# Kernel optimization log

Hardware: AMD Instinct MI355X
Metric: run time of the kernel (lower is better)

Reference implementation:

```python
import jax, jax.numpy as jnp
import numpy as np

B, FIN, FOUT, FH2, NMIX, LAT, H, W = 16, 256, 256, 256, 8, 512, 64, 64


def _xavier(key, shape):
    # xavier_normal_ over last-two-ish dims; simple fan-based scale
    fan_in = int(np.prod(shape[1:]))
    fan_out = shape[0]
    s = (2.0 / (fan_in + fan_out)) ** 0.5
    return jax.random.normal(key, shape, jnp.float32) * s


def setup_inputs() -> dict:
    key = jax.random.key(0)
    ks = jax.random.split(key, 12)
    return {
        "x": jax.random.normal(ks[0], (B, FIN, H, W), jnp.float32),
        "lat": jax.random.normal(ks[1], (B, LAT), jnp.float32),
        # mixture kernel banks [n_mix, out_ch, in_ch] (kernel_size=1 squeezed)
        "k_in_mix": _xavier(ks[2], (NMIX, FH2, FIN)),
        "k_mid_mix": _xavier(ks[3], (NMIX, FH2, 2 * FH2)),
        "k_out_mix": _xavier(ks[4], (NMIX, FOUT, 2 * FH2)),
        "k_short_mix": _xavier(ks[5], (NMIX, FOUT, FIN)),
        # mixture bias banks [n_mix, ch]
        "b_in_mix": _xavier(ks[6], (NMIX, FH2)),
        "b_mid_mix": _xavier(ks[7], (NMIX, FH2)),
        "b_out_mix": _xavier(ks[8], (NMIX, FOUT)),
        "b_short_mix": _xavier(ks[9], (NMIX, FOUT)),
        # dyna_mix = nn.Linear(lat_size, n_mix) (lat_factor=0 path)
        "w_dyna": _xavier(ks[10], (NMIX, LAT)),
        "b_dyna": jnp.zeros((NMIX,), jnp.float32),
    }


def _complex_wave(h):
    # doubles channel dim: concat(sin, cos) along channels (per sample)
    return jnp.concatenate([jnp.sin(h), jnp.cos(h)], axis=1)


def reference(x, lat, k_in_mix, k_mid_mix, k_out_mix, k_short_mix,
              b_in_mix, b_mid_mix, b_out_mix, b_short_mix, w_dyna, b_dyna):
    # mixing coefficients per sample: [B, n_mix]
    mix = lat @ w_dyna.T + b_dyna
    # per-sample 1x1 conv kernels via mixture reduction: [B, out, in]
    k_in = jnp.einsum('bm,moi->boi', mix, k_in_mix)
    k_mid = jnp.einsum('bm,moi->boi', mix, k_mid_mix)
    k_out = jnp.einsum('bm,moi->boi', mix, k_out_mix)
    k_short = jnp.einsum('bm,moi->boi', mix, k_short_mix)
    # per-sample biases: [B, ch, 1, 1]
    b_in = (mix @ b_in_mix)[:, :, None, None]
    b_mid = (mix @ b_mid_mix)[:, :, None, None]
    b_out = (mix @ b_out_mix)[:, :, None, None]
    b_short = (mix @ b_short_mix)[:, :, None, None]
    # grouped conv with groups = batch (kernel_size=1) == per-sample matmul
    short = jnp.einsum('boi,bihw->bohw', k_short, x) + b_short
    h = jnp.einsum('boi,bihw->bohw', k_in, x) + b_in            # [B, FH2, H, W]
    h = _complex_wave(h)                                        # [B, 2*FH2, H, W]
    h = jnp.einsum('boi,bihw->bohw', k_mid, h) + b_mid
    h = _complex_wave(h)
    out = jnp.einsum('boi,bihw->bohw', k_out, h) + b_out + short
    return out
```

## Files before the change

### kernel.cpp

```cpp
#include <hip/hip_runtime.h>
#include <stdint.h>

#define B_    16
#define FIN   256
#define FOUT  256
#define FH2   256
#define NMIX  8
#define LAT   512
#define HW    4096
#define MT    64

typedef short bf16x8 __attribute__((ext_vector_type(8)));
typedef float f32x4  __attribute__((ext_vector_type(4)));

#define WS_MIX    0
#define WS_BIAS   1024
#define WS_WIN    131072
#define WS_WMID   2228224
#define WS_WOUT   6422528
#define WS_WSHORT 10616832

__device__ __forceinline__ uint16_t f2bf(float f) {
  uint32_t u = __builtin_bit_cast(uint32_t, f);
  u += 0x7fffu + ((u >> 16) & 1u);
  return (uint16_t)(u >> 16);
}
__device__ __forceinline__ uint32_t pack2(float lo, float hi) {
  return (uint32_t)f2bf(lo) | ((uint32_t)f2bf(hi) << 16);
}

#define MFMA(a, b, c) __builtin_amdgcn_mfma_f32_16x16x32_bf16(a, b, c, 0, 0, 0)

__global__ void k_mix_bias(const float* __restrict__ lat,
                           const float* __restrict__ w_dyna,
                           const float* __restrict__ b_dyna,
                           const float* __restrict__ b_in_mix,
                           const float* __restrict__ b_mid_mix,
                           const float* __restrict__ b_out_mix,
                           const float* __restrict__ b_short_mix,
                           float* __restrict__ ws_mix,
                           float* __restrict__ ws_bias) {
  __shared__ float smix[NMIX];
  const int t = threadIdx.x;
  const int lane = t & 63, wv = t >> 6;
  const int b = blockIdx.x;
#pragma unroll
  for (int d2 = 0; d2 < 2; d2++) {
    int m = wv * 2 + d2;
    float s = 0.f;
#pragma unroll
    for (int j = 0; j < 8; j++)
      s += lat[b * LAT + j * 64 + lane] * w_dyna[m * LAT + j * 64 + lane];
#pragma unroll
    for (int off = 32; off; off >>= 1) s += __shfl_xor(s, off);
    if (lane == 0) {
      float v = s + b_dyna[m];
      ws_mix[b * NMIX + m] = v;
      smix[m] = v;
    }
  }
  __syncthreads();
  const float* banks[4] = {b_in_mix, b_mid_mix, b_out_mix, b_short_mix};
  for (int pos = t; pos < 1024; pos += 256) {
    int bank = pos >> 8, ch = pos & 255;
    const float* bp = banks[bank];
    float a = 0.f;
#pragma unroll
    for (int m = 0; m < NMIX; m++) a += smix[m] * bp[m * 256 + ch];
    ws_bias[(bank * B_ + b) * 256 + ch] = a;
  }
}

__global__ void k_weights(const float* __restrict__ k_in_mix,
                          const float* __restrict__ k_mid_mix,
                          const float* __restrict__ k_out_mix,
                          const float* __restrict__ k_short_mix,
                          const float* __restrict__ ws_mix,
                          uint16_t* __restrict__ w_in,
                          uint16_t* __restrict__ w_mid,
                          uint16_t* __restrict__ w_out,
                          uint16_t* __restrict__ w_short) {
  __shared__ float smix[B_ * NMIX];
  const int t = threadIdx.x;
  if (t < B_ * NMIX) smix[t] = ws_mix[t];
  __syncthreads();
  const int e8 = (blockIdx.x * 256 + t) * 8;
  const float* srcA;
  uint16_t* dst;
  int sstride, dstride;
  bool ileave;
  if (e8 < 65536) {
    int e = e8;
    int lane = (e >> 3) & 63, ots = (e >> 9) & 3, kt = (e >> 11) & 7, wv = e >> 14;
    int row = wv * 64 + ots * 16 + (lane & 15);
    int k0 = kt * 32 + (lane >> 4) * 8;
    srcA = k_in_mix + row * 256 + k0; sstride = 65536; ileave = false;
    dst = w_in + e;                   dstride = 65536;
  } else if (e8 < 196608) {
    int e = e8 - 65536;
    int lane = (e >> 3) & 63, ots = (e >> 9) & 3, kt = (e >> 11) & 15, wv = e >> 15;
    int row = wv * 64 + ots * 16 + (lane & 15);
    int kp0 = kt * 32 + (lane >> 4) * 8;
    srcA = k_mid_mix + row * 512 + (kp0 >> 1); sstride = 131072; ileave = true;
    dst = w_mid + e;                           dstride = 131072;
  } else if (e8 < 327680) {
    int e = e8 - 196608;
    int lane = (e >> 3) & 63, ots = (e >> 9) & 3, kt = (e >> 11) & 15, wv = e >> 15;
    int row = wv * 64 + ots * 16 + (lane & 15);
    int kp0 = kt * 32 + (lane >> 4) * 8;
    srcA = k_out_mix + row * 512 + (kp0 >> 1); sstride = 131072; ileave = true;
    dst = w_out + e;                           dstride = 131072;
  } else {
    int e = e8 - 327680;
    int lane = (e >> 3) & 63, ots = (e >> 9) & 3, kt = (e >> 11) & 7, wv = e >> 14;
    int row = wv * 64 + ots * 16 + (lane & 15);
    int k0 = kt * 32 + (lane >> 4) * 8;
    srcA = k_short_mix + row * 256 + k0; sstride = 65536; ileave = false;
    dst = w_short + e;                   dstride = 65536;
  }
  const int boff = ileave ? 256 : 4;
  float4 va[NMIX], vb[NMIX];
#pragma unroll
  for (int m = 0; m < NMIX; m++) {
    va[m] = *(const float4*)(srcA + m * sstride);
    vb[m] = *(const float4*)(srcA + m * sstride + boff);
  }
  for (int b = 0; b < B_; b++) {
    float4 ra = make_float4(0.f, 0.f, 0.f, 0.f), rb = ra;
#pragma unroll
    for (int m = 0; m < NMIX; m++) {
      const float s = smix[b * NMIX + m];
      ra.x += s * va[m].x; ra.y += s * va[m].y; ra.z += s * va[m].z; ra.w += s * va[m].w;
      rb.x += s * vb[m].x; rb.y += s * vb[m].y; rb.z += s * vb[m].z; rb.w += s * vb[m].w;
    }
    int4 pkt;
    if (ileave) {
      pkt = make_int4((int)pack2(ra.x, rb.x), (int)pack2(ra.y, rb.y),
                      (int)pack2(ra.z, rb.z), (int)pack2(ra.w, rb.w));
    } else {
      pkt = make_int4((int)pack2(ra.x, ra.y), (int)pack2(ra.z, ra.w),
                      (int)pack2(rb.x, rb.y), (int)pack2(rb.z, rb.w));
    }
    *(int4*)(dst + (size_t)b * dstride) = pkt;
  }
}

__launch_bounds__(256, 2)
__global__ void k_main(const float* __restrict__ x,
                       const float* __restrict__ ws_bias,
                       const uint16_t* __restrict__ w_in,
                       const uint16_t* __restrict__ w_mid,
                       const uint16_t* __restrict__ w_out,
                       const uint16_t* __restrict__ w_short,
                       float* __restrict__ out) {
  __shared__ int4 smem4[81920 / 16];
  char* lds = (char*)smem4;
  char* Xc = lds;
  char* H1 = lds + 16384;

  const int t = threadIdx.x;
  const int lane = t & 63;
  const int wv = t >> 6;
  const int q = lane >> 4;
  const int n = lane & 15;
  const int b = blockIdx.x & 15;
  const int p0 = (blockIdx.x >> 4) * MT;

  const float* xb = x + (size_t)b * FIN * HW + p0;
  const int xpos = t & 63;

  float xv[2][8];
#pragma unroll
  for (int u = 0; u < 2; u++) {
    const int cg = wv * 2 + u;
#pragma unroll
    for (int e = 0; e < 8; e++)
      xv[u][e] = xb[(size_t)(cg * 8 + e) * HW + xpos];
  }
#pragma unroll
  for (int u = 0; u < 2; u++) {
    const int cg = wv * 2 + u;
    *(int4*)(Xc + xpos * 128 + ((cg ^ (xpos & 7)) * 16)) =
        make_int4((int)pack2(xv[u][0], xv[u][1]), (int)pack2(xv[u][2], xv[u][3]),
                  (int)pack2(xv[u][4], xv[u][5]), (int)pack2(xv[u][6], xv[u][7]));
  }

  f32x4 acc_h[4][4], acc_s[4][4];
#pragma unroll
  for (int ots = 0; ots < 4; ots++) {
    const int o = wv * 64 + ots * 16 + q * 4;
    const float4 vi = *(const float4*)&ws_bias[(0 * B_ + b) * 256 + o];
    const float4 vs = *(const float4*)&ws_bias[(3 * B_ + b) * 256 + o];
    f32x4 ah, asv;
    ah[0] = vi.x; ah[1] = vi.y; ah[2] = vi.z; ah[3] = vi.w;
    asv[0] = vs.x; asv[1] = vs.y; asv[2] = vs.z; asv[3] = vs.w;
#pragma unroll
    for (int pt = 0; pt < 4; pt++) { acc_h[ots][pt] = ah; acc_s[ots][pt] = asv; }
  }

  const uint16_t* Wi = w_in + (size_t)b * 65536 + wv * 16384 + lane * 8;
  const uint16_t* Ws = w_short + (size_t)b * 65536 + wv * 16384 + lane * 8;
  bf16x8 ai[2][4], asf[2][4];
#pragma unroll
  for (int ots = 0; ots < 4; ots++) {
    ai[0][ots] = *(const bf16x8*)(Wi + ots * 512);
    asf[0][ots] = *(const bf16x8*)(Ws + ots * 512);
  }
  __syncthreads();

#pragma unroll
  for (int c = 0; c < 4; c++) {
    if (c < 3) {
#pragma unroll
      for (int u = 0; u < 2; u++) {
        const int cg = wv * 2 + u;
#pragma unroll
        for (int e = 0; e < 8; e++)
          xv[u][e] = xb[(size_t)((c + 1) * 64 + cg * 8 + e) * HW + xpos];
      }
    }
    const char* Xr = Xc + (c & 1) * 8192;
#pragma unroll
    for (int lh = 0; lh < 2; lh++) {
      const int kt = c * 2 + lh;
      if (kt < 7) {
#pragma unroll
        for (int ots = 0; ots < 4; ots++) {
          ai[(kt + 1) & 1][ots] = *(const bf16x8*)(Wi + (kt + 1) * 2048 + ots * 512);
          asf[(kt + 1) & 1][ots] = *(const bf16x8*)(Ws + (kt + 1) * 2048 + ots * 512);
        }
      }
      bf16x8 bf[4];
#pragma unroll
      for (int pt = 0; pt < 4; pt++) {
        const int p = pt * 16 + n;
        bf[pt] = *(const bf16x8*)(Xr + p * 128 + (((lh * 4 + q) ^ (p & 7)) * 16));
      }
      __builtin_amdgcn_s_setprio(1);
#pragma unroll
      for (int ots = 0; ots < 4; ots++) {
#pragma unroll
        for (int pt = 0; pt < 4; pt++) {
          acc_h[ots][pt] = MFMA(ai[kt & 1][ots], bf[pt], acc_h[ots][pt]);
          acc_s[ots][pt] = MFMA(asf[kt & 1][ots], bf[pt], acc_s[ots][pt]);
        }
      }
      __builtin_amdgcn_s_setprio(0);
    }
    if (c < 3) {
#pragma unroll
      for (int u = 0; u < 2; u++) {
        const int cg = wv * 2 + u;
        *(int4*)(Xc + ((c + 1) & 1) * 8192 + xpos * 128 + ((cg ^ (xpos & 7)) * 16)) =
            make_int4((int)pack2(xv[u][0], xv[u][1]), (int)pack2(xv[u][2], xv[u][3]),
                      (int)pack2(xv[u][4], xv[u][5]), (int)pack2(xv[u][6], xv[u][7]));
      }
      __syncthreads();
    }
  }

#pragma unroll
  for (int ots = 0; ots < 4; ots++) {
    const int ctile = (wv * 4 + ots) * 4 + q;
#pragma unroll
    for (int pt = 0; pt < 4; pt++) {
      const int p = pt * 16 + n;
      *(int4*)(H1 + p * 1024 + ((ctile ^ (p & 7)) * 16)) = make_int4(
          (int)pack2(__sinf(acc_h[ots][pt][0]), __cosf(acc_h[ots][pt][0])),
          (int)pack2(__sinf(acc_h[ots][pt][1]), __cosf(acc_h[ots][pt][1])),
          (int)pack2(__sinf(acc_h[ots][pt][2]), __cosf(acc_h[ots][pt][2])),
          (int)pack2(__sinf(acc_h[ots][pt][3]), __cosf(acc_h[ots][pt][3])));
    }
  }

  const uint16_t* Wm = w_mid + (size_t)b * 131072 + wv * 32768 + lane * 8;
  bf16x8 am[4][4];
#pragma unroll
  for (int ots = 0; ots < 4; ots++) {
    am[0][ots] = *(const bf16x8*)(Wm + 0 * 2048 + ots * 512);
    am[1][ots] = *(const bf16x8*)(Wm + 1 * 2048 + ots * 512);
    am[2][ots] = *(const bf16x8*)(Wm + 2 * 2048 + ots * 512);
  }
  f32x4 acc2[4][4];
#pragma unroll
  for (int ots = 0; ots < 4; ots++) {
    const int o = wv * 64 + ots * 16 + q * 4;
    const float4 v = *(const float4*)&ws_bias[(1 * B_ + b) * 256 + o];
    f32x4 a2;
    a2[0] = v.x; a2[1] = v.y; a2[2] = v.z; a2[3] = v.w;
#pragma unroll
    for (int pt = 0; pt < 4; pt++) acc2[ots][pt] = a2;
  }
  __syncthreads();

  {
    bf16x8 bfB[2][4];
#pragma unroll
    for (int pt = 0; pt < 4; pt++) {
      const int p = pt * 16 + n;
      bfB[0][pt] = *(const bf16x8*)(H1 + p * 1024 + ((q ^ (p & 7)) * 16));
    }
#pragma unroll
    for (int kt = 0; kt < 16; kt++) {
      if (kt < 15) {
#pragma unroll
        for (int pt = 0; pt < 4; pt++) {
          const int p = pt * 16 + n;
          bfB[(kt + 1) & 1][pt] =
              *(const bf16x8*)(H1 + p * 1024 + ((((kt + 1) * 4 + q) ^ (p & 7)) * 16));
        }
      }
      if (kt < 13) {
#pragma unroll
        for (int ots = 0; ots < 4; ots++)
          am[(kt + 3) & 3][ots] = *(const bf16x8*)(Wm + (kt + 3) * 2048 + ots * 512);
      }
      __builtin_amdgcn_s_setprio(1);
#pragma unroll
      for (int ots = 0; ots < 4; ots++)
#pragma unroll
        for (int pt = 0; pt < 4; pt++)
          acc2[ots][pt] = MFMA(am[kt & 3][ots], bfB[kt & 1][pt], acc2[ots][pt]);
      __builtin_amdgcn_s_setprio(0);
    }
  }
  __syncthreads();

#pragma unroll
  for (int ots = 0; ots < 4; ots++) {
    const int ctile = (wv * 4 + ots) * 4 + q;
#pragma unroll
    for (int pt = 0; pt < 4; pt++) {
      const int p = pt * 16 + n;
      *(int4*)(H1 + p * 1024 + ((ctile ^ (p & 7)) * 16)) = make_int4(
          (int)pack2(__sinf(acc2[ots][pt][0]), __cosf(acc2[ots][pt][0])),
          (int)pack2(__sinf(acc2[ots][pt][1]), __cosf(acc2[ots][pt][1])),
          (int)pack2(__sinf(acc2[ots][pt][2]), __cosf(acc2[ots][pt][2])),
          (int)pack2(__sinf(acc2[ots][pt][3]), __cosf(acc2[ots][pt][3])));
    }
  }

  const uint16_t* Wo = w_out + (size_t)b * 131072 + wv * 32768 + lane * 8;
  bf16x8 ao[4][4];
#pragma unroll
  for (int ots = 0; ots < 4; ots++) {
    ao[0][ots] = *(const bf16x8*)(Wo + 0 * 2048 + ots * 512);
    ao[1][ots] = *(const bf16x8*)(Wo + 1 * 2048 + ots * 512);
    ao[2][ots] = *(const bf16x8*)(Wo + 2 * 2048 + ots * 512);
  }
#pragma unroll
  for (int ots = 0; ots < 4; ots++) {
    const int o = wv * 64 + ots * 16 + q * 4;
    const float4 v = *(const float4*)&ws_bias[(2 * B_ + b) * 256 + o];
#pragma unroll
    for (int pt = 0; pt < 4; pt++) {
      acc_s[ots][pt][0] += v.x; acc_s[ots][pt][1] += v.y;
      acc_s[ots][pt][2] += v.z; acc_s[ots][pt][3] += v.w;
    }
  }
  __syncthreads();

  {
    bf16x8 bfC[2][4];
#pragma unroll
    for (int pt = 0; pt < 4; pt++) {
      const int p = pt * 16 + n;
      bfC[0][pt] = *(const bf16x8*)(H1 + p * 1024 + ((q ^ (p & 7)) * 16));
    }
#pragma unroll
    for (int kt = 0; kt < 16; kt++) {
      if (kt < 15) {
#pragma unroll
        for (int pt = 0; pt < 4; pt++) {
          const int p = pt * 16 + n;
          bfC[(kt + 1) & 1][pt] =
              *(const bf16x8*)(H1 + p * 1024 + ((((kt + 1) * 4 + q) ^ (p & 7)) * 16));
        }
      }
      if (kt < 13) {
#pragma unroll
        for (int ots = 0; ots < 4; ots++)
          ao[(kt + 3) & 3][ots] = *(const bf16x8*)(Wo + (kt + 3) * 2048 + ots * 512);
      }
      __builtin_amdgcn_s_setprio(1);
#pragma unroll
      for (int ots = 0; ots < 4; ots++)
#pragma unroll
        for (int pt = 0; pt < 4; pt++)
          acc_s[ots][pt] = MFMA(ao[kt & 3][ots], bfC[kt & 1][pt], acc_s[ots][pt]);
      __builtin_amdgcn_s_setprio(0);
    }
  }

  {
    float* ob = out + (size_t)b * FOUT * HW + p0;
#pragma unroll
    for (int ots = 0; ots < 4; ots++) {
#pragma unroll
      for (int pt = 0; pt < 4; pt++) {
#pragma unroll
        for (int r = 0; r < 4; r++) {
          const int o = wv * 64 + ots * 16 + q * 4 + r;
          ob[(size_t)o * HW + pt * 16 + n] = acc_s[ots][pt][r];
        }
      }
    }
  }
}

extern "C" void kernel_launch(void* const* d_in, const int* in_sizes, int n_in,
                              void* d_out, int out_size, void* d_ws, size_t ws_size,
                              hipStream_t stream) {
  const float* x           = (const float*)d_in[0];
  const float* lat         = (const float*)d_in[1];
  const float* k_in_mix    = (const float*)d_in[2];
  const float* k_mid_mix   = (const float*)d_in[3];
  const float* k_out_mix   = (const float*)d_in[4];
  const float* k_short_mix = (const float*)d_in[5];
  const float* b_in_mix    = (const float*)d_in[6];
  const float* b_mid_mix   = (const float*)d_in[7];
  const float* b_out_mix   = (const float*)d_in[8];
  const float* b_short_mix = (const float*)d_in[9];
  const float* w_dyna      = (const float*)d_in[10];
  const float* b_dyna      = (const float*)d_in[11];

  char* ws = (char*)d_ws;
  float*    ws_mix  = (float*)(ws + WS_MIX);
  float*    ws_bias = (float*)(ws + WS_BIAS);
  uint16_t* w_in    = (uint16_t*)(ws + WS_WIN);
  uint16_t* w_mid   = (uint16_t*)(ws + WS_WMID);
  uint16_t* w_out   = (uint16_t*)(ws + WS_WOUT);
  uint16_t* w_short = (uint16_t*)(ws + WS_WSHORT);
  float* out = (float*)d_out;

  hipLaunchKernelGGL(k_mix_bias, dim3(16), dim3(256), 0, stream,
                     lat, w_dyna, b_dyna, b_in_mix, b_mid_mix, b_out_mix,
                     b_short_mix, ws_mix, ws_bias);
  hipLaunchKernelGGL(k_weights, dim3(192), dim3(256), 0, stream,
                     k_in_mix, k_mid_mix, k_out_mix, k_short_mix, ws_mix,
                     w_in, w_mid, w_out, w_short);
  hipLaunchKernelGGL(k_main, dim3(1024), dim3(256), 0, stream,
                     x, ws_bias, w_in, w_mid, w_out, w_short, out);
}
```

Before: 212.8 us.

## Load full X tile up front, alias H1 over X, shrink weight prefetch depth

The first GEMM no longer streams X in four double-buffered chunks. Each thread loads all 64 input channels up front and writes the full 32KB bf16 X tile to LDS, which then shares storage with the H1 buffer, cutting LDS from 80KB to 64KB. The mid and out GEMM weight prefetch drops from a 3-deep to a 2-deep register ring, issued after the MFMAs. The aim is fewer barriers, lower LDS use and lower register pressure, at the cost of a large serialized global load before any compute and less latency hiding for weight loads.

```diff
diff --git a/kernel.cpp b/kernel.cpp
--- a/kernel.cpp
+++ b/kernel.cpp
@@ -153,10 +153,10 @@
                        const uint16_t* __restrict__ w_out,
                        const uint16_t* __restrict__ w_short,
                        float* __restrict__ out) {
-  __shared__ int4 smem4[81920 / 16];
+  __shared__ int4 smem4[65536 / 16];
   char* lds = (char*)smem4;
-  char* Xc = lds;
-  char* H1 = lds + 16384;
+  char* Xs = lds;
+  char* H1 = lds;
 
   const int t = threadIdx.x;
   const int lane = t & 63;
@@ -169,20 +169,22 @@
   const float* xb = x + (size_t)b * FIN * HW + p0;
   const int xpos = t & 63;
 
-  float xv[2][8];
-#pragma unroll
-  for (int u = 0; u < 2; u++) {
-    const int cg = wv * 2 + u;
-#pragma unroll
-    for (int e = 0; e < 8; e++)
-      xv[u][e] = xb[(size_t)(cg * 8 + e) * HW + xpos];
-  }
-#pragma unroll
-  for (int u = 0; u < 2; u++) {
-    const int cg = wv * 2 + u;
-    *(int4*)(Xc + xpos * 128 + ((cg ^ (xpos & 7)) * 16)) =
-        make_int4((int)pack2(xv[u][0], xv[u][1]), (int)pack2(xv[u][2], xv[u][3]),
-                  (int)pack2(xv[u][4], xv[u][5]), (int)pack2(xv[u][6], xv[u][7]));
+  {
+    float xr[8][8];
+#pragma unroll
+    for (int u = 0; u < 8; u++) {
+      const int cg = wv * 8 + u;
+#pragma unroll
+      for (int e = 0; e < 8; e++)
+        xr[u][e] = xb[(size_t)(cg * 8 + e) * HW + xpos];
+    }
+#pragma unroll
+    for (int u = 0; u < 8; u++) {
+      const int cg = wv * 8 + u;
+      *(int4*)(Xs + xpos * 512 + ((cg ^ (xpos & 7)) * 16)) = make_int4(
+          (int)pack2(xr[u][0], xr[u][1]), (int)pack2(xr[u][2], xr[u][3]),
+          (int)pack2(xr[u][4], xr[u][5]), (int)pack2(xr[u][6], xr[u][7]));
+    }
   }
 
   f32x4 acc_h[4][4], acc_s[4][4];
@@ -209,55 +211,32 @@
   __syncthreads();
 
 #pragma unroll
-  for (int c = 0; c < 4; c++) {
-    if (c < 3) {
-#pragma unroll
-      for (int u = 0; u < 2; u++) {
-        const int cg = wv * 2 + u;
-#pragma unroll
-        for (int e = 0; e < 8; e++)
-          xv[u][e] = xb[(size_t)((c + 1) * 64 + cg * 8 + e) * HW + xpos];
-      }
-    }
-    const char* Xr = Xc + (c & 1) * 8192;
-#pragma unroll
-    for (int lh = 0; lh < 2; lh++) {
-      const int kt = c * 2 + lh;
-      if (kt < 7) {
-#pragma unroll
-        for (int ots = 0; ots < 4; ots++) {
-          ai[(kt + 1) & 1][ots] = *(const bf16x8*)(Wi + (kt + 1) * 2048 + ots * 512);
-          asf[(kt + 1) & 1][ots] = *(const bf16x8*)(Ws + (kt + 1) * 2048 + ots * 512);
-        }
-      }
-      bf16x8 bf[4];
+  for (int kt = 0; kt < 8; kt++) {
+    if (kt < 7) {
+#pragma unroll
+      for (int ots = 0; ots < 4; ots++) {
+        ai[(kt + 1) & 1][ots] = *(const bf16x8*)(Wi + (kt + 1) * 2048 + ots * 512);
+        asf[(kt + 1) & 1][ots] = *(const bf16x8*)(Ws + (kt + 1) * 2048 + ots * 512);
+      }
+    }
+    bf16x8 bf[4];
+#pragma unroll
+    for (int pt = 0; pt < 4; pt++) {
+      const int p = pt * 16 + n;
+      bf[pt] = *(const bf16x8*)(Xs + p * 512 + (((kt * 4 + q) ^ (p & 7)) * 16));
+    }
+    __builtin_amdgcn_s_setprio(1);
+#pragma unroll
+    for (int ots = 0; ots < 4; ots++) {
 #pragma unroll
       for (int pt = 0; pt < 4; pt++) {
-        const int p = pt * 16 + n;
-        bf[pt] = *(const bf16x8*)(Xr + p * 128 + (((lh * 4 + q) ^ (p & 7)) * 16));
-      }
-      __builtin_amdgcn_s_setprio(1);
-#pragma unroll
-      for (int ots = 0; ots < 4; ots++) {
-#pragma unroll
-        for (int pt = 0; pt < 4; pt++) {
-          acc_h[ots][pt] = MFMA(ai[kt & 1][ots], bf[pt], acc_h[ots][pt]);
-          acc_s[ots][pt] = MFMA(asf[kt & 1][ots], bf[pt], acc_s[ots][pt]);
-        }
-      }
-      __builtin_amdgcn_s_setprio(0);
-    }
-    if (c < 3) {
-#pragma unroll
-      for (int u = 0; u < 2; u++) {
-        const int cg = wv * 2 + u;
-        *(int4*)(Xc + ((c + 1) & 1) * 8192 + xpos * 128 + ((cg ^ (xpos & 7)) * 16)) =
-            make_int4((int)pack2(xv[u][0], xv[u][1]), (int)pack2(xv[u][2], xv[u][3]),
-                      (int)pack2(xv[u][4], xv[u][5]), (int)pack2(xv[u][6], xv[u][7]));
-      }
-      __syncthreads();
-    }
-  }
+        acc_h[ots][pt] = MFMA(ai[kt & 1][ots], bf[pt], acc_h[ots][pt]);
+        acc_s[ots][pt] = MFMA(asf[kt & 1][ots], bf[pt], acc_s[ots][pt]);
+      }
+    }
+    __builtin_amdgcn_s_setprio(0);
+  }
+  __syncthreads();
 
 #pragma unroll
   for (int ots = 0; ots < 4; ots++) {
@@ -274,12 +253,11 @@
   }
 
   const uint16_t* Wm = w_mid + (size_t)b * 131072 + wv * 32768 + lane * 8;
-  bf16x8 am[4][4];
+  bf16x8 am[2][4];
 #pragma unroll
   for (int ots = 0; ots < 4; ots++) {
     am[0][ots] = *(const bf16x8*)(Wm + 0 * 2048 + ots * 512);
     am[1][ots] = *(const bf16x8*)(Wm + 1 * 2048 + ots * 512);
-    am[2][ots] = *(const bf16x8*)(Wm + 2 * 2048 + ots * 512);
   }
   f32x4 acc2[4][4];
 #pragma unroll
@@ -294,11 +272,11 @@
   __syncthreads();
 
   {
-    bf16x8 bfB[2][4];
+    bf16x8 bfP[2][4];
 #pragma unroll
     for (int pt = 0; pt < 4; pt++) {
       const int p = pt * 16 + n;
-      bfB[0][pt] = *(const bf16x8*)(H1 + p * 1024 + ((q ^ (p & 7)) * 16));
+      bfP[0][pt] = *(const bf16x8*)(H1 + p * 1024 + ((q ^ (p & 7)) * 16));
     }
 #pragma unroll
     for (int kt = 0; kt < 16; kt++) {
@@ -306,22 +284,22 @@
 #pragma unroll
         for (int pt = 0; pt < 4; pt++) {
           const int p = pt * 16 + n;
-          bfB[(kt + 1) & 1][pt] =
+          bfP[(kt + 1) & 1][pt] =
               *(const bf16x8*)(H1 + p * 1024 + ((((kt + 1) * 4 + q) ^ (p & 7)) * 16));
         }
       }
-      if (kt < 13) {
+      __builtin_amdgcn_s_setprio(1);
+#pragma unroll
+      for (int ots = 0; ots < 4; ots++)
+#pragma unroll
+        for (int pt = 0; pt < 4; pt++)
+          acc2[ots][pt] = MFMA(am[kt & 1][ots], bfP[kt & 1][pt], acc2[ots][pt]);
+      __builtin_amdgcn_s_setprio(0);
+      if (kt < 14) {
 #pragma unroll
         for (int ots = 0; ots < 4; ots++)
-          am[(kt + 3) & 3][ots] = *(const bf16x8*)(Wm + (kt + 3) * 2048 + ots * 512);
-      }
-      __builtin_amdgcn_s_setprio(1);
-#pragma unroll
-      for (int ots = 0; ots < 4; ots++)
-#pragma unroll
-        for (int pt = 0; pt < 4; pt++)
-          acc2[ots][pt] = MFMA(am[kt & 3][ots], bfB[kt & 1][pt], acc2[ots][pt]);
-      __builtin_amdgcn_s_setprio(0);
+          am[kt & 1][ots] = *(const bf16x8*)(Wm + (kt + 2) * 2048 + ots * 512);
+      }
     }
   }
   __syncthreads();
@@ -341,12 +319,11 @@
   }
 
   const uint16_t* Wo = w_out + (size_t)b * 131072 + wv * 32768 + lane * 8;
-  bf16x8 ao[4][4];
+  bf16x8 ao[2][4];
 #pragma unroll
   for (int ots = 0; ots < 4; ots++) {
     ao[0][ots] = *(const bf16x8*)(Wo + 0 * 2048 + ots * 512);
     ao[1][ots] = *(const bf16x8*)(Wo + 1 * 2048 + ots * 512);
-    ao[2][ots] = *(const bf16x8*)(Wo + 2 * 2048 + ots * 512);
   }
 #pragma unroll
   for (int ots = 0; ots < 4; ots++) {
@@ -361,11 +338,11 @@
   __syncthreads();
 
   {
-    bf16x8 bfC[2][4];
+    bf16x8 bfP[2][4];
 #pragma unroll
     for (int pt = 0; pt < 4; pt++) {
       const int p = pt * 16 + n;
-      bfC[0][pt] = *(const bf16x8*)(H1 + p * 1024 + ((q ^ (p & 7)) * 16));
+      bfP[0][pt] = *(const bf16x8*)(H1 + p * 1024 + ((q ^ (p & 7)) * 16));
     }
 #pragma unroll
     for (int kt = 0; kt < 16; kt++) {
@@ -373,22 +350,22 @@
 #pragma unroll
         for (int pt = 0; pt < 4; pt++) {
           const int p = pt * 16 + n;
-          bfC[(kt + 1) & 1][pt] =
+          bfP[(kt + 1) & 1][pt] =
               *(const bf16x8*)(H1 + p * 1024 + ((((kt + 1) * 4 + q) ^ (p & 7)) * 16));
         }
       }
-      if (kt < 13) {
+      __builtin_amdgcn_s_setprio(1);
+#pragma unroll
+      for (int ots = 0; ots < 4; ots++)
+#pragma unroll
+        for (int pt = 0; pt < 4; pt++)
+          acc_s[ots][pt] = MFMA(ao[kt & 1][ots], bfP[kt & 1][pt], acc_s[ots][pt]);
+      __builtin_amdgcn_s_setprio(0);
+      if (kt < 14) {
 #pragma unroll
         for (int ots = 0; ots < 4; ots++)
-          ao[(kt + 3) & 3][ots] = *(const bf16x8*)(Wo + (kt + 3) * 2048 + ots * 512);
-      }
-      __builtin_amdgcn_s_setprio(1);
-#pragma unroll
-      for (int ots = 0; ots < 4; ots++)
-#pragma unroll
-        for (int pt = 0; pt < 4; pt++)
-          acc_s[ots][pt] = MFMA(ao[kt & 3][ots], bfC[kt & 1][pt], acc_s[ots][pt]);
-      __builtin_amdgcn_s_setprio(0);
+          ao[kt & 1][ots] = *(const bf16x8*)(Wo + (kt + 2) * 2048 + ots * 512);
+      }
     }
   }
 
```

Result: faster. 190.3 us (-10.6%).
